# Optimization experiments

Measured on AMD Instinct MI355X. Metric: run time of the kernel, lower is better.

The kernel has to match this reference:

```python
import jax, jax.numpy as jnp
import numpy as np

H = W = 256
N_VERTS = 6890
N_FACES = 13776
CHUNK = 164            # 13776 = 84 * 164
N_CHUNKS = N_FACES // CHUNK
BIG = 1e9
EPS = 1e-8


def _project(cam, verts):
    # weak-perspective: s * (xy + t); flip y into image (raster) space
    xy = cam[:, None, 0:1] * (verts[:, :, :2] + cam[:, None, 1:3])
    return jnp.concatenate([xy[..., 0:1], -xy[..., 1:2], verts[:, :, 2:3]], axis=-1)  # [B,N,3]


def _rasterize(proj, faces):
    """Z-buffered rasterization. proj [B,N,3], faces [F,3] ->
    fim [B,P] int32 (face index, -1 = background), wim [B,P,3] barycentric weights."""
    B = proj.shape[0]
    P = H * W
    tri = proj[:, faces]                                   # [B,F,3,3]
    tri_c = tri.reshape(B, N_CHUNKS, CHUNK, 3, 3).transpose(1, 0, 2, 3, 4)  # [nc,B,C,3,3]
    bases = (jnp.arange(N_CHUNKS) * CHUNK).astype(jnp.int32)
    c = (jnp.arange(H, dtype=jnp.float32) + 0.5) / H * 2.0 - 1.0   # pixel centers in [-1,1]
    py, px = jnp.meshgrid(c, c, indexing='ij')
    px = px.reshape(-1)[None, :, None]                     # [1,P,1]
    py = py.reshape(-1)[None, :, None]

    def step(carry, xs):
        zbuf, fid, wim = carry
        t, base = xs                                       # t [B,CHUNK,3,3]
        v = t[:, None]                                     # [B,1,CHUNK,3,3]
        x0, y0, z0 = v[..., 0, 0], v[..., 0, 1], v[..., 0, 2]
        x1, y1, z1 = v[..., 1, 0], v[..., 1, 1], v[..., 1, 2]
        x2, y2, z2 = v[..., 2, 0], v[..., 2, 1], v[..., 2, 2]
        denom = (y1 - y2) * (x0 - x2) + (x2 - x1) * (y0 - y2)
        inv = 1.0 / jnp.where(jnp.abs(denom) < EPS, 1.0, denom)
        w0 = ((y1 - y2) * (px - x2) + (x2 - x1) * (py - y2)) * inv   # [B,P,CHUNK]
        w1 = ((y2 - y0) * (px - x2) + (x0 - x2) * (py - y2)) * inv
        w2 = 1.0 - w0 - w1
        inside = (w0 >= 0) & (w1 >= 0) & (w2 >= 0) & (jnp.abs(denom) >= EPS)
        depth = jnp.where(inside, w0 * z0 + w1 * z1 + w2 * z2, BIG)
        loc = jnp.argmin(depth, axis=-1)                   # [B,P]
        li = loc[..., None]
        dmin = jnp.take_along_axis(depth, li, -1)[..., 0]
        b0 = jnp.take_along_axis(w0, li, -1)[..., 0]
        b1 = jnp.take_along_axis(w1, li, -1)[..., 0]
        b2 = jnp.take_along_axis(w2, li, -1)[..., 0]
        bsel = jnp.stack([b0, b1, b2], axis=-1)            # [B,P,3]
        upd = dmin < zbuf
        zbuf = jnp.where(upd, dmin, zbuf)
        fid = jnp.where(upd, base + loc.astype(jnp.int32), fid)
        wim = jnp.where(upd[..., None], bsel, wim)
        return (zbuf, fid, wim), None

    init = (jnp.full((B, P), BIG, jnp.float32),
            jnp.full((B, P), -1, jnp.int32),
            jnp.zeros((B, P, 3), jnp.float32))
    (zbuf, fid, wim), _ = jax.lax.scan(step, init, (tri_c, bases))
    return fid, wim


def _grid_sample_border(img, grid):
    # torch.nn.functional.grid_sample(bilinear, padding_mode='border', align_corners=False)
    B, C, Hh, Ww = img.shape
    ix = jnp.clip(((grid[..., 0] + 1.0) * Ww - 1.0) * 0.5, 0.0, Ww - 1.0)
    iy = jnp.clip(((grid[..., 1] + 1.0) * Hh - 1.0) * 0.5, 0.0, Hh - 1.0)
    x0 = jnp.floor(ix); y0 = jnp.floor(iy)
    wx = ix - x0; wy = iy - y0
    x0i = x0.astype(jnp.int32); y0i = y0.astype(jnp.int32)
    x1i = jnp.clip(x0i + 1, 0, Ww - 1); y1i = jnp.clip(y0i + 1, 0, Hh - 1)
    b = jnp.arange(B)[:, None, None]
    Ia = img[b, :, y0i, x0i]   # [B,H,W,C]
    Ib = img[b, :, y0i, x1i]
    Ic = img[b, :, y1i, x0i]
    Id = img[b, :, y1i, x1i]
    out = (Ia * ((1 - wx) * (1 - wy))[..., None] + Ib * (wx * (1 - wy))[..., None]
           + Ic * ((1 - wx) * wy)[..., None] + Id * (wx * wy)[..., None])
    return out.transpose(0, 3, 1, 2)


def setup_inputs() -> dict:
    key = jax.random.key(0)
    k1, k2, k3, k4, k5, k6 = jax.random.split(key, 6)
    B = 2
    return {
        'src_img': jax.random.normal(k1, (B, 3, H, W), jnp.float32),
        'src_cam': jax.random.uniform(k2, (B, 3), jnp.float32),
        'src_vertices': jax.random.normal(k3, (B, N_VERTS, 3), jnp.float32),
        'tgt_cam': jax.random.uniform(k4, (B, 3), jnp.float32),
        'tgt_vertices': jax.random.normal(k5, (B, N_VERTS, 3), jnp.float32),
        'faces': jax.random.randint(k6, (N_FACES, 3), 0, N_VERTS, jnp.int32),
    }


def reference(src_img, src_cam, src_vertices, tgt_cam, tgt_vertices, faces):
    B = src_img.shape[0]
    # source faces -> projected 2D verts; flip y back (matches src_f2verts[...,1] *= -1)
    src_proj = _project(src_cam, src_vertices)
    src_f2v = src_proj[:, faces][..., 0:2]                 # [B,F,3,2]
    src_f2v = src_f2v.at[..., 1].multiply(-1.0)
    # rasterize target mesh -> face-index map + barycentric weight map
    tgt_proj = _project(tgt_cam, tgt_vertices)
    fim, wim = _rasterize(tgt_proj, faces)                 # [B,P], [B,P,3]
    fid_clip = jnp.clip(fim, 0, N_FACES - 1)
    gathered = src_f2v[jnp.arange(B)[:, None], fid_clip]   # [B,P,3,2]
    flow = jnp.sum(wim[..., None] * gathered, axis=2)      # [B,P,2]
    flow = jnp.where((fim >= 0)[..., None], flow, -2.0)    # background off-grid
    flow = flow.reshape(B, H, W, 2)
    return _grid_sample_border(src_img, flow)
```

## Files before the change

kernel.cpp:

```cpp
#include <hip/hip_runtime.h>

#pragma clang fp contract(off)

#define HH 256
#define WW 256
#define NVERTS 6890
#define NFACES 13776
#define RASTN (NFACES + 1)
#define PAD1 14336
#define LISTSTRIDE 13824
#define RCHUNK 32
#define MAXCH 432
#define KSPLIT 16
#define SLABS 4
#define WSUB 896
#define NITER 14
#define SLABSZ (4 * WSUB)
#define NBLK 2048
#define NWAVES (NBLK * 4)
#define BIGF 1000000000.0f
#define EPSF 1e-8f

__device__ __forceinline__ float pixc(int i) {
    return __fsub_rn(__fmul_rn(__fdiv_rn(__fadd_rn((float)i, 0.5f), 256.0f), 2.0f), 1.0f);
}

__device__ __forceinline__ unsigned int fsort(float f) {
    unsigned int u = __float_as_uint(f);
    return (u & 0x80000000u) ? ~u : (u | 0x80000000u);
}

__device__ __forceinline__ float funsort(unsigned int u) {
    if (u == 0xFFFFFFFFu) return BIGF;
    unsigned int v = (u & 0x80000000u) ? (u & 0x7FFFFFFFu) : ~u;
    return __uint_as_float(v);
}


__global__ __launch_bounds__(256) void precompute_kernel(
    const float* __restrict__ src_cam, const float* __restrict__ src_verts,
    const float* __restrict__ tgt_cam, const float* __restrict__ tgt_verts,
    const int* __restrict__ faces,
    float4* __restrict__ rast64, float* __restrict__ fz,
    uchar4* __restrict__ pass1,
    float4* __restrict__ eplane,
    float4* __restrict__ flowg,
    unsigned long long* __restrict__ zbuf,
    int* __restrict__ counts, int* __restrict__ done,
    int* __restrict__ qcountA, int* __restrict__ qcountB,
    int B)
{
    int idx = blockIdx.x * blockDim.x + threadIdx.x;
    if (idx < B * HH * WW) zbuf[idx] = ~0ull;
    if (counts && idx < B * 256) { counts[idx] = 0; done[idx] = 0; }
    if (qcountA && idx == 0) { qcountA[0] = 0; qcountB[0] = 0; }
    if (idx >= B * PAD1) return;
    int b = idx / PAD1;
    int f = idx - b * PAD1;
    if (f >= NFACES) {
        if (pass1) pass1[(size_t)b * PAD1 + f] = make_uchar4(255, 255, 0, 0);
        if (f == NFACES) {
            float4* rr = rast64 + ((size_t)b * RASTN + f) * 4;
            rr[0] = make_float4(0.0f, 0.0f, 0.0f, 0.0f);
            rr[1] = make_float4(0.0f, 0.0f, 1.0f, __int_as_float(-1));
            rr[2] = make_float4(BIGF, BIGF, BIGF, 0.0f);
            rr[3] = make_float4(0.0f, 0.0f, 0.0f, 0.0f);
            if (fz) fz[(size_t)b * RASTN + f] = BIGF;
        }
        return;
    }
    float4* rr = rast64 + ((size_t)b * RASTN + f) * 4;
    int i0 = faces[3*f+0], i1 = faces[3*f+1], i2 = faces[3*f+2];

    float tc0 = tgt_cam[3*b+0], tc1 = tgt_cam[3*b+1], tc2 = tgt_cam[3*b+2];
    const float* tv = tgt_verts + (size_t)b * NVERTS * 3;
    float x0 = __fmul_rn(tc0, __fadd_rn(tv[3*i0+0], tc1));
    float y0 = -__fmul_rn(tc0, __fadd_rn(tv[3*i0+1], tc2));
    float z0 = tv[3*i0+2];
    float x1 = __fmul_rn(tc0, __fadd_rn(tv[3*i1+0], tc1));
    float y1 = -__fmul_rn(tc0, __fadd_rn(tv[3*i1+1], tc2));
    float z1 = tv[3*i1+2];
    float x2 = __fmul_rn(tc0, __fadd_rn(tv[3*i2+0], tc1));
    float y2 = -__fmul_rn(tc0, __fadd_rn(tv[3*i2+1], tc2));
    float z2 = tv[3*i2+2];

    float A  = __fsub_rn(y1, y2);
    float D  = __fsub_rn(x0, x2);
    float Bc = __fsub_rn(x2, x1);
    float E_ = __fsub_rn(y0, y2);
    float denom = __fadd_rn(__fmul_rn(A, D), __fmul_rn(Bc, E_));
    bool valid = (fabsf(denom) >= EPSF);
    float inv = __fdiv_rn(1.0f, valid ? denom : 1.0f);
    float Cc = __fsub_rn(y2, y0);

    float fzmin = fminf(fminf(z0, z1), z2)
                - 4e-6f * (fabsf(z0) + fabsf(z1) + fabsf(z2)) - 1e-30f;

    if (valid) {
        rr[0] = make_float4(x2, y2, A, Bc);
        rr[1] = make_float4(Cc, D, inv, __int_as_float(f));
        rr[2] = make_float4(z0, z1, z2, 0.0f);
    } else {
        rr[0] = make_float4(0.0f, 0.0f, 0.0f, 0.0f);
        rr[1] = make_float4(0.0f, 0.0f, 1.0f, __int_as_float(f));
        rr[2] = make_float4(BIGF, BIGF, BIGF, 0.0f);
    }
    rr[3] = make_float4(0.0f, 0.0f, 0.0f, 0.0f);
    if (fz) fz[(size_t)b * RASTN + f] = valid ? fzmin : BIGF;

    uchar4 range;
    float4 e1, e2, e3;
    if (valid) {
        float xmn = fminf(fminf(x0, x1), x2), xmx = fmaxf(fmaxf(x0, x1), x2);
        float ymn = fminf(fminf(y0, y1), y2), ymx = fmaxf(fmaxf(y0, y1), y2);
        float S = fmaxf(fmaxf(fabsf(xmn), fabsf(xmx)),
                        fmaxf(fabsf(ymn), fabsf(ymx))) + 1.01f;
        float slop = 2e-6f * S;
        float l0 = sqrtf(D*D + E_*E_);
        float dx1v = x1 - x2, dy1v = y1 - y2;
        float l1 = sqrtf(dx1v*dx1v + dy1v*dy1v);
        float dx2v = x1 - x0, dy2v = y1 - y0;
        float l2 = sqrtf(dx2v*dx2v + dy2v*dy2v);
        float mp = fmaxf(fmaxf(l0*l1, l1*l2), l0*l2);
        float Ex = slop * mp / fabsf(denom);
        float m = Ex + slop + 1e-4f;
        float bxmn = xmn - m, bymn = ymn - m, bxmx = xmx + m, bymx = ymx + m;

        int txlo = (int)floorf((__fmul_rn(__fadd_rn(bxmn, 1.0f), 128.0f) - 15.5f) * 0.0625f);
        txlo = max(0, min(16, txlo));
        while (txlo > 0  && pixc(16*(txlo-1)+15) >= bxmn) txlo--;
        while (txlo < 16 && pixc(16*txlo+15)     <  bxmn) txlo++;
        int txhi = (int)floorf((__fmul_rn(__fadd_rn(bxmx, 1.0f), 128.0f) - 0.5f) * 0.0625f);
        txhi = max(-1, min(15, txhi));
        while (txhi < 15 && pixc(16*(txhi+1)) <= bxmx) txhi++;
        while (txhi >= 0 && pixc(16*txhi)     >  bxmx) txhi--;
        int tylo = (int)floorf((__fmul_rn(__fadd_rn(bymn, 1.0f), 128.0f) - 15.5f) * 0.0625f);
        tylo = max(0, min(16, tylo));
        while (tylo > 0  && pixc(16*(tylo-1)+15) >= bymn) tylo--;
        while (tylo < 16 && pixc(16*tylo+15)     <  bymn) tylo++;
        int tyhi = (int)floorf((__fmul_rn(__fadd_rn(bymx, 1.0f), 128.0f) - 0.5f) * 0.0625f);
        tyhi = max(-1, min(15, tyhi));
        while (tyhi < 15 && pixc(16*(tyhi+1)) <= bymx) tyhi++;
        while (tyhi >= 0 && pixc(16*tyhi)     >  bymx) tyhi--;
        if (txlo > txhi || tylo > tyhi || txlo > 15 || tylo > 15 ||
            txhi < 0 || tyhi < 0) {
            range = make_uchar4(255, 255, 0, 0);
        } else {
            range = make_uchar4((unsigned char)txlo, (unsigned char)tylo,
                                (unsigned char)txhi, (unsigned char)tyhi);
        }

        float s = (denom >= 0.0f) ? 1.0f : -1.0f;
        float gx0 = s * A,  gy0 = s * Bc;
        float gx1 = s * Cc, gy1 = s * D;
        float gx2 = s * (y0 - y1), gy2 = s * (x1 - x0);
        float b0 = -(gx0 * x2 + gy0 * y2);
        float b1 = -(gx1 * x2 + gy1 * y2);
        float b2 = fabsf(denom) - b0 - b1;
        float mm15 = 1.5f * m;
        float k0 = b0 + mm15 * l1 + 1e-6f;
        float k1 = b1 + mm15 * l0 + 1e-6f;
        float k2 = b2 + mm15 * l2 + 1e-6f;
        e1 = make_float4(gx0, gy0, k0, gx1);
        e2 = make_float4(gy1, k1, gx2, gy2);
        e3 = make_float4(k2, 0.0f, 0.0f, 0.0f);
    } else {
        range = make_uchar4(255, 255, 0, 0);
        e1 = make_float4(0.0f, 0.0f, -1.0f, 0.0f);
        e2 = make_float4(0.0f, -1.0f, 0.0f, 0.0f);
        e3 = make_float4(-1.0f, 0.0f, 0.0f, 0.0f);
    }
    if (pass1) pass1[(size_t)b * PAD1 + f] = range;
    if (eplane) {
        float4* ep = eplane + ((size_t)b * NFACES + f) * 4;
        ep[0] = e1; ep[1] = e2; ep[2] = e3;
        ep[3] = make_float4(0.0f, 0.0f, 0.0f, 0.0f);
    }

    float sc0 = src_cam[3*b+0], sc1 = src_cam[3*b+1], sc2 = src_cam[3*b+2];
    const float* sv = src_verts + (size_t)b * NVERTS * 3;
    float g0x = __fmul_rn(sc0, __fadd_rn(sv[3*i0+0], sc1));
    float g0y = __fmul_rn(sc0, __fadd_rn(sv[3*i0+1], sc2));
    float g1x = __fmul_rn(sc0, __fadd_rn(sv[3*i1+0], sc1));
    float g1y = __fmul_rn(sc0, __fadd_rn(sv[3*i1+1], sc2));
    float g2x = __fmul_rn(sc0, __fadd_rn(sv[3*i2+0], sc1));
    float g2y = __fmul_rn(sc0, __fadd_rn(sv[3*i2+1], sc2));
    size_t fo = ((size_t)b * NFACES + f) * 2;
    flowg[fo+0] = make_float4(g0x, g0y, g1x, g1y);
    flowg[fo+1] = make_float4(g2x, g2y, 0.0f, 0.0f);
}

__global__ __launch_bounds__(256) void bin_kernel(
    const uchar4* __restrict__ pass1, const float4* __restrict__ eplane,
    int* __restrict__ lists,
    int* __restrict__ counts, int* __restrict__ done,
    unsigned int* __restrict__ queueA, int* __restrict__ qcountA,
    unsigned int* __restrict__ queueB, int* __restrict__ qcountB, int B)
{
    __shared__ int seg[4][WSUB];
    int tile = blockIdx.x;
    int slab = blockIdx.y;
    int b = blockIdx.z;
    int tileG = b * 256 + tile;
    int tX = tile & 15, tY = tile >> 4;
    float txmin = pixc(tX * 16), txmax = pixc(tX * 16 + 15);
    float tymin = pixc(tY * 16), tymax = pixc(tY * 16 + 15);

    int wv = threadIdx.x >> 6, lane = threadIdx.x & 63;
    const uchar4* p1 = pass1 + (size_t)b * PAD1;
    const float4* ep = eplane + (size_t)b * NFACES * 4;
    int* mylist = lists + (size_t)tileG * LISTSTRIDE;
    int wlo = slab * SLABSZ + wv * WSUB;
    int cnt = 0;

    int f0 = wlo + lane;
    uchar4 c = p1[f0];

    #pragma unroll
    for (int it = 0; it < NITER; ++it) {
        uchar4 n;
        if (it + 1 < NITER) n = p1[f0 + (it + 1) * 64];
        int f = f0 + it * 64;
        bool pass = (tX >= (int)c.x) & (tX <= (int)c.z) &
                    (tY >= (int)c.y) & (tY <= (int)c.w);
        unsigned long long m = __ballot(pass);
        if (pass) {
            int pre = __popcll(m & ((1ull << lane) - 1ull));
            seg[wv][cnt + pre] = f;
        }
        cnt += __popcll(m);
        c = n;
    }

    int outc = 0;
    for (int base = 0; base < cnt; base += 64) {
        int i = base + lane;
        int f = (i < cnt) ? seg[wv][i] : 0;
        const float4* er = ep + (size_t)f * 4;
        float4 e1 = er[0], e2 = er[1], e3 = er[2];
        float v0 = e1.x * (e1.x >= 0.0f ? txmax : txmin)
                 + e1.y * (e1.y >= 0.0f ? tymax : tymin) + e1.z;
        float v1 = e1.w * (e1.w >= 0.0f ? txmax : txmin)
                 + e2.x * (e2.x >= 0.0f ? tymax : tymin) + e2.y;
        float v2 = e2.z * (e2.z >= 0.0f ? txmax : txmin)
                 + e2.w * (e2.w >= 0.0f ? tymax : tymin) + e3.x;
        bool pass = (i < cnt) & (v0 >= 0.0f) & (v1 >= 0.0f) & (v2 >= 0.0f);
        unsigned long long m = __ballot(pass);
        if (pass) {
            int pre = __popcll(m & ((1ull << lane) - 1ull));
            seg[wv][outc + pre] = f;
        }
        outc += __popcll(m);
    }
    cnt = outc;

    int gbase = 0;
    if (lane == 0 && cnt) gbase = atomicAdd(&counts[tileG], cnt);
    gbase = __shfl(gbase, 0);
    for (int i = lane; i < cnt; i += 64) mylist[gbase + i] = seg[wv][i];

    __syncthreads();
    if (threadIdx.x < 64) {
        int isLast = 0, cc = 0;
        if (threadIdx.x == 0) {
            isLast = (atomicAdd(&done[tileG], 1) == SLABS - 1);
            if (isLast) cc = atomicAdd(&counts[tileG], 0);
        }
        isLast = __shfl(isLast, 0);
        if (isLast) {
            cc = __shfl(cc, 0);
            int padded = (cc + RCHUNK - 1) & ~(RCHUNK - 1);
            for (int i = cc + threadIdx.x; i < padded; i += 64)
                mylist[i] = NFACES;
            int nch = padded / RCHUNK;
            int na = min(nch, KSPLIT);
            int nb = nch - na;
            if (na) {
                int qb = 0;
                if (threadIdx.x == 0) qb = atomicAdd(qcountA, na);
                qb = __shfl(qb, 0);
                for (int kk = threadIdx.x; kk < na; kk += 64)
                    queueA[qb + kk] =
                        ((unsigned int)tileG << 10) | (unsigned int)kk;
            }
            if (nb) {
                int qb = 0;
                if (threadIdx.x == 0) qb = atomicAdd(qcountB, nb);
                qb = __shfl(qb, 0);
                for (int kk = threadIdx.x; kk < nb; kk += 64)
                    queueB[qb + kk] =
                        ((unsigned int)tileG << 10) | (unsigned int)(KSPLIT + kk);
            }
        }
    }
}

__global__ __launch_bounds__(256) void raster_kernel(
    const float* __restrict__ rast64, const int* __restrict__ lists,
    const float* __restrict__ fz,
    const unsigned int* __restrict__ queue, const int* __restrict__ qcount,
    unsigned long long* __restrict__ zbuf, int B, int cull)
{
    int wv = threadIdx.x >> 6, lane = threadIdx.x & 63;
    int waveId = blockIdx.x * 4 + wv;
    int qn = queue ? qcount[0] : B * 256 * MAXCH;
    qn = __builtin_amdgcn_readfirstlane(qn);

    for (int e = waveId; e < qn; e += NWAVES) {
        int tileG, k;
        if (queue) {
            unsigned int ent = queue[e];
            tileG = (int)(ent >> 10); k = (int)(ent & 1023u);
        } else {
            tileG = e / MAXCH; k = e - tileG * MAXCH;
        }
        tileG = __builtin_amdgcn_readfirstlane(tileG);
        k = __builtin_amdgcn_readfirstlane(k);
        const int* lp = lists ? (lists + (size_t)tileG * LISTSTRIDE + k * RCHUNK)
                              : nullptr;
        int b = tileG >> 8, tile = tileG & 255;
        const float* rb = rast64 + (size_t)b * RASTN * 16;

        int tX = tile & 15, tY = tile >> 4;
        int col = lane & 15, row0 = lane >> 4;
        int pxi = tX * 16 + col;
        float px = pixc(pxi);
        int ry0 = tY * 16 + row0;
        float py0 = pixc(ry0);
        float py1 = pixc(ry0 + 4);
        float py2 = pixc(ry0 + 8);
        float py3 = pixc(ry0 + 12);

        float z0c = BIGF, z1c = BIGF, z2c = BIGF, z3c = BIGF;
        int f0c = -1, f1c = -1, f2c = -1, f3c = -1;

        if (cull && lp) {
            size_t zbase = ((size_t)b << 16) | (size_t)pxi;
            unsigned long long pk0 = zbuf[zbase | ((size_t)ry0 << 8)];
            unsigned long long pk1 = zbuf[zbase | ((size_t)(ry0 + 4) << 8)];
            unsigned long long pk2 = zbuf[zbase | ((size_t)(ry0 + 8) << 8)];
            unsigned long long pk3 = zbuf[zbase | ((size_t)(ry0 + 12) << 8)];
            float lb = fmaxf(fmaxf(funsort((unsigned int)(pk0 >> 32)),
                                   funsort((unsigned int)(pk1 >> 32))),
                             fmaxf(funsort((unsigned int)(pk2 >> 32)),
                                   funsort((unsigned int)(pk3 >> 32))));
            #pragma unroll
            for (int off = 1; off < 64; off <<= 1)
                lb = fmaxf(lb, __shfl_xor(lb, off, 64));
            int fidx = lp[lane & 31];
            float fzv = fz[(size_t)b * RASTN + fidx];
            unsigned long long bm = __ballot((lane < 32) & (fzv <= lb));
            unsigned int mask = (unsigned int)bm;
            if (mask == 0u) continue;

            for (int j = 0; j < RCHUNK; j += 4) {
                unsigned int g = (mask >> j) & 0xFu;
                if (!g) continue;
                int4 fis = *(const int4*)(lp + j);
                #pragma unroll
                for (int q = 0; q < 4; ++q) {
                    if (!(g & (1u << q))) continue;
                    int fi = (q == 0) ? fis.x : (q == 1) ? fis.y
                           : (q == 2) ? fis.z : fis.w;
                    fi = __builtin_amdgcn_readfirstlane(fi);
                    const float* r = rb + (size_t)fi * 16;
                    float X2 = r[0], Y2 = r[1], A = r[2], Bc = r[3];
                    float Cc = r[4], Dd = r[5], inv = r[6];
                    int   fid = __float_as_int(r[7]);
                    float Z0 = r[8], Z1 = r[9], Z2 = r[10];
                    float dx  = __fsub_rn(px, X2);
                    float Adx = __fmul_rn(A, dx);
                    float Cdx = __fmul_rn(Cc, dx);
                    auto evalp = [&](float py, float& zc, int& fc) {
                        float dy = __fsub_rn(py, Y2);
                        float w0 = __fmul_rn(__fadd_rn(Adx, __fmul_rn(Bc, dy)), inv);
                        float w1 = __fmul_rn(__fadd_rn(Cdx, __fmul_rn(Dd, dy)), inv);
                        float w2 = __fsub_rn(__fsub_rn(1.0f, w0), w1);
                        float d  = __fadd_rn(__fadd_rn(__fmul_rn(w0, Z0),
                                                       __fmul_rn(w1, Z1)),
                                             __fmul_rn(w2, Z2));
                        float mm = fminf(fminf(w0, w1), w2);
                        bool ins = (mm >= 0.0f) & (d < zc);
                        if (ins) { zc = d; fc = fid; }
                    };
                    evalp(py0, z0c, f0c);
                    evalp(py1, z1c, f1c);
                    evalp(py2, z2c, f2c);
                    evalp(py3, z3c, f3c);
                }
            }
        } else {
            for (int j = 0; j < RCHUNK; j += 4) {
                int4 fis;
                if (lp) {
                    fis = *(const int4*)(lp + j);
                } else {
                    int base = k * RCHUNK + j;
                    fis.x = min(base + 0, NFACES); fis.y = min(base + 1, NFACES);
                    fis.z = min(base + 2, NFACES); fis.w = min(base + 3, NFACES);
                }
                #pragma unroll
                for (int q = 0; q < 4; ++q) {
                    int fi = (q == 0) ? fis.x : (q == 1) ? fis.y
                           : (q == 2) ? fis.z : fis.w;
                    fi = __builtin_amdgcn_readfirstlane(fi);
                    const float* r = rb + (size_t)fi * 16;
                    float X2 = r[0], Y2 = r[1], A = r[2], Bc = r[3];
                    float Cc = r[4], Dd = r[5], inv = r[6];
                    int   fid = __float_as_int(r[7]);
                    float Z0 = r[8], Z1 = r[9], Z2 = r[10];
                    float dx  = __fsub_rn(px, X2);
                    float Adx = __fmul_rn(A, dx);
                    float Cdx = __fmul_rn(Cc, dx);
                    auto evalp = [&](float py, float& zc, int& fc) {
                        float dy = __fsub_rn(py, Y2);
                        float w0 = __fmul_rn(__fadd_rn(Adx, __fmul_rn(Bc, dy)), inv);
                        float w1 = __fmul_rn(__fadd_rn(Cdx, __fmul_rn(Dd, dy)), inv);
                        float w2 = __fsub_rn(__fsub_rn(1.0f, w0), w1);
                        float d  = __fadd_rn(__fadd_rn(__fmul_rn(w0, Z0),
                                                       __fmul_rn(w1, Z1)),
                                             __fmul_rn(w2, Z2));
                        float mm = fminf(fminf(w0, w1), w2);
                        bool ins = (mm >= 0.0f) & (d < zc);
                        if (ins) { zc = d; fc = fid; }
                    };
                    evalp(py0, z0c, f0c);
                    evalp(py1, z1c, f1c);
                    evalp(py2, z2c, f2c);
                    evalp(py3, z3c, f3c);
                }
            }
        }

        auto commit = [&](int rowk, float zc, int fc) {
            if (fc >= 0) {
                unsigned long long pk =
                    ((unsigned long long)fsort(zc) << 32) | (unsigned int)fc;
                int pyi = ry0 + rowk * 4;
                atomicMin(&zbuf[((size_t)b << 16) | (pyi << 8) | pxi], pk);
            }
        };
        commit(0, z0c, f0c);
        commit(1, z1c, f1c);
        commit(2, z2c, f2c);
        commit(3, z3c, f3c);
    }
}

__global__ __launch_bounds__(256) void resolve_kernel(
    const float* __restrict__ rast64, const float4* __restrict__ flowg,
    const unsigned long long* __restrict__ zbuf,
    const float* __restrict__ src_img, float* __restrict__ out, int B)
{
    int idx = blockIdx.x * 256 + threadIdx.x;
    if (idx >= B * HH * WW) return;
    int b = idx >> 16;
    int pix = idx & 65535;
    int pxi = pix & 255, pyi = pix >> 8;
    float px = pixc(pxi), py = pixc(pyi);

    unsigned int fid = (unsigned int)zbuf[idx];
    float fx, fy;
    if (fid != 0xFFFFFFFFu) {
        const float* r = rast64 + ((size_t)b * RASTN + fid) * 16;
        float dx = __fsub_rn(px, r[0]);
        float dy = __fsub_rn(py, r[1]);
        float w0 = __fmul_rn(__fadd_rn(__fmul_rn(r[2], dx), __fmul_rn(r[3], dy)), r[6]);
        float w1 = __fmul_rn(__fadd_rn(__fmul_rn(r[4], dx), __fmul_rn(r[5], dy)), r[6]);
        float w2 = __fsub_rn(__fsub_rn(1.0f, w0), w1);
        const float4* fg = flowg + ((size_t)b * NFACES + fid) * 2;
        float4 g0 = fg[0];
        float4 g1 = fg[1];
        fx = __fadd_rn(__fadd_rn(__fmul_rn(w0, g0.x), __fmul_rn(w1, g0.z)),
                       __fmul_rn(w2, g1.x));
        fy = __fadd_rn(__fadd_rn(__fmul_rn(w0, g0.y), __fmul_rn(w1, g0.w)),
                       __fmul_rn(w2, g1.y));
    } else {
        fx = -2.0f; fy = -2.0f;
    }

    float ix = __fmul_rn(__fsub_rn(__fmul_rn(__fadd_rn(fx, 1.0f), 256.0f), 1.0f), 0.5f);
    float iy = __fmul_rn(__fsub_rn(__fmul_rn(__fadd_rn(fy, 1.0f), 256.0f), 1.0f), 0.5f);
    ix = fminf(fmaxf(ix, 0.0f), 255.0f);
    iy = fminf(fmaxf(iy, 0.0f), 255.0f);
    float x0f = floorf(ix), y0f = floorf(iy);
    float wx = __fsub_rn(ix, x0f), wy = __fsub_rn(iy, y0f);
    int x0i = (int)x0f, y0i = (int)y0f;
    int x1i = min(x0i + 1, 255), y1i = min(y0i + 1, 255);
    float omwx = __fsub_rn(1.0f, wx), omwy = __fsub_rn(1.0f, wy);
    float wa = __fmul_rn(omwx, omwy);
    float wb = __fmul_rn(wx, omwy);
    float wc = __fmul_rn(omwx, wy);
    float wd = __fmul_rn(wx, wy);
    const float* img = src_img + (size_t)b * 3 * HH * WW;
    int o00 = y0i * WW + x0i, o01 = y0i * WW + x1i;
    int o10 = y1i * WW + x0i, o11 = y1i * WW + x1i;
    float* ob = out + (size_t)b * 3 * HH * WW + (size_t)pyi * WW + pxi;
    for (int c = 0; c < 3; ++c) {
        const float* ic = img + (size_t)c * HH * WW;
        float Ia = ic[o00], Ib = ic[o01], Ic = ic[o10], Id = ic[o11];
        float val = __fadd_rn(__fadd_rn(__fadd_rn(__fmul_rn(Ia, wa), __fmul_rn(Ib, wb)),
                                        __fmul_rn(Ic, wc)),
                              __fmul_rn(Id, wd));
        ob[(size_t)c * HH * WW] = val;
    }
}

extern "C" void kernel_launch(void* const* d_in, const int* in_sizes, int n_in,
                              void* d_out, int out_size, void* d_ws, size_t ws_size,
                              hipStream_t stream)
{
    const float* src_img   = (const float*)d_in[0];
    const float* src_cam   = (const float*)d_in[1];
    const float* src_verts = (const float*)d_in[2];
    const float* tgt_cam   = (const float*)d_in[3];
    const float* tgt_verts = (const float*)d_in[4];
    const int*   faces     = (const int*)d_in[5];
    int B = in_sizes[1] / 3;

    size_t off = 0;
    auto alloc = [&](size_t bytes) {
        size_t o = off;
        off = (off + bytes + 255) & ~(size_t)255;
        return o;
    };
    size_t rastOff = alloc((size_t)B * RASTN * 64);
    size_t fzOff   = alloc((size_t)B * RASTN * sizeof(float));
    size_t p1Off   = alloc((size_t)B * PAD1 * 4);
    size_t edgOff  = alloc((size_t)B * NFACES * 64);
    size_t flowOff = alloc((size_t)B * NFACES * 2 * sizeof(float4));
    size_t zbufOff = alloc((size_t)B * HH * WW * sizeof(unsigned long long));
    size_t cntOff  = alloc((size_t)B * 256 * sizeof(int));
    size_t donOff  = alloc((size_t)B * 256 * sizeof(int));
    size_t qcAOff  = alloc(sizeof(int));
    size_t qcBOff  = alloc(sizeof(int));
    size_t quAOff  = alloc((size_t)B * 256 * KSPLIT * sizeof(unsigned int));
    size_t quBOff  = alloc((size_t)B * 256 * MAXCH * sizeof(unsigned int));
    size_t listOff = alloc((size_t)B * 256 * LISTSTRIDE * sizeof(int));
    bool binned = (off <= ws_size);

    char* ws = (char*)d_ws;
    float4* rast64 = (float4*)(ws + rastOff);
    float*  fz     = (float*)(ws + fzOff);
    uchar4* pass1  = binned ? (uchar4*)(ws + p1Off)  : nullptr;
    float4* eplane = binned ? (float4*)(ws + edgOff) : nullptr;
    float4* flowg  = (float4*)(ws + flowOff);
    unsigned long long* zbuf = (unsigned long long*)(ws + zbufOff);
    int* counts = binned ? (int*)(ws + cntOff) : nullptr;
    int* done   = binned ? (int*)(ws + donOff) : nullptr;
    int* qcountA = binned ? (int*)(ws + qcAOff) : nullptr;
    int* qcountB = binned ? (int*)(ws + qcBOff) : nullptr;
    unsigned int* queueA = binned ? (unsigned int*)(ws + quAOff) : nullptr;
    unsigned int* queueB = binned ? (unsigned int*)(ws + quBOff) : nullptr;
    int* lists  = binned ? (int*)(ws + listOff) : nullptr;

    int nInit = B * HH * WW;
    int nPre  = B * PAD1;
    int nMax  = nInit > nPre ? nInit : nPre;
    precompute_kernel<<<(nMax + 255) / 256, 256, 0, stream>>>(
        src_cam, src_verts, tgt_cam, tgt_verts, faces,
        rast64, fz, pass1, eplane, flowg, zbuf, counts, done,
        qcountA, qcountB, B);
    if (binned) {
        bin_kernel<<<dim3(256, SLABS, B), 256, 0, stream>>>(
            pass1, eplane, lists, counts, done,
            queueA, qcountA, queueB, qcountB, B);
        raster_kernel<<<NBLK, 256, 0, stream>>>(
            (const float*)rast64, lists, fz, queueA, qcountA, zbuf, B, 0);
        raster_kernel<<<NBLK, 256, 0, stream>>>(
            (const float*)rast64, lists, fz, queueB, qcountB, zbuf, B, 1);
    } else {
        raster_kernel<<<NBLK, 256, 0, stream>>>(
            (const float*)rast64, nullptr, fz, nullptr, nullptr, zbuf, B, 0);
    }
    resolve_kernel<<<(B * HH * WW + 255) / 256, 256, 0, stream>>>(
        (const float*)rast64, flowg, zbuf, src_img, (float*)d_out, B);
}
```

Before: 140.1 us.

## Replace tile-parallel binning with face-parallel count/prefix/scatter binning

```diff
diff --git a/kernel.cpp b/kernel.cpp
--- a/kernel.cpp
+++ b/kernel.cpp
@@ -7,17 +7,13 @@
 #define NVERTS 6890
 #define NFACES 13776
 #define RASTN (NFACES + 1)
-#define PAD1 14336
 #define LISTSTRIDE 13824
 #define RCHUNK 32
 #define MAXCH 432
 #define KSPLIT 16
-#define SLABS 4
-#define WSUB 896
-#define NITER 14
-#define SLABSZ (4 * WSUB)
 #define NBLK 2048
 #define NWAVES (NBLK * 4)
+#define MAXB 4
 #define BIGF 1000000000.0f
 #define EPSF 1e-8f
 
@@ -42,34 +38,27 @@
     const float* __restrict__ tgt_cam, const float* __restrict__ tgt_verts,
     const int* __restrict__ faces,
     float4* __restrict__ rast64, float* __restrict__ fz,
-    uchar4* __restrict__ pass1,
-    float4* __restrict__ eplane,
+    float4* __restrict__ binrec,
     float4* __restrict__ flowg,
     unsigned long long* __restrict__ zbuf,
-    int* __restrict__ counts, int* __restrict__ done,
     int* __restrict__ qcountA, int* __restrict__ qcountB,
     int B)
 {
     int idx = blockIdx.x * blockDim.x + threadIdx.x;
     if (idx < B * HH * WW) zbuf[idx] = ~0ull;
-    if (counts && idx < B * 256) { counts[idx] = 0; done[idx] = 0; }
     if (qcountA && idx == 0) { qcountA[0] = 0; qcountB[0] = 0; }
-    if (idx >= B * PAD1) return;
-    int b = idx / PAD1;
-    int f = idx - b * PAD1;
-    if (f >= NFACES) {
-        if (pass1) pass1[(size_t)b * PAD1 + f] = make_uchar4(255, 255, 0, 0);
-        if (f == NFACES) {
-            float4* rr = rast64 + ((size_t)b * RASTN + f) * 4;
-            rr[0] = make_float4(0.0f, 0.0f, 0.0f, 0.0f);
-            rr[1] = make_float4(0.0f, 0.0f, 1.0f, __int_as_float(-1));
-            rr[2] = make_float4(BIGF, BIGF, BIGF, 0.0f);
-            rr[3] = make_float4(0.0f, 0.0f, 0.0f, 0.0f);
-            if (fz) fz[(size_t)b * RASTN + f] = BIGF;
-        }
+    if (idx >= B * RASTN) return;
+    int b = idx / RASTN;
+    int f = idx - b * RASTN;
+    float4* rr = rast64 + ((size_t)b * RASTN + f) * 4;
+    if (f == NFACES) {
+        rr[0] = make_float4(0.0f, 0.0f, 0.0f, 0.0f);
+        rr[1] = make_float4(0.0f, 0.0f, 1.0f, __int_as_float(-1));
+        rr[2] = make_float4(BIGF, BIGF, BIGF, 0.0f);
+        rr[3] = make_float4(0.0f, 0.0f, 0.0f, 0.0f);
+        if (fz) fz[(size_t)b * RASTN + f] = BIGF;
         return;
     }
-    float4* rr = rast64 + ((size_t)b * RASTN + f) * 4;
     int i0 = faces[3*f+0], i1 = faces[3*f+1], i2 = faces[3*f+2];
 
     float tc0 = tgt_cam[3*b+0], tc1 = tgt_cam[3*b+1], tc2 = tgt_cam[3*b+2];
@@ -108,8 +97,9 @@
     rr[3] = make_float4(0.0f, 0.0f, 0.0f, 0.0f);
     if (fz) fz[(size_t)b * RASTN + f] = valid ? fzmin : BIGF;
 
-    uchar4 range;
-    float4 e1, e2, e3;
+    unsigned int rngbits = 255u | (255u << 8);
+    float4 e1, e2;
+    float k2v = -1.0f;
     if (valid) {
         float xmn = fminf(fminf(x0, x1), x2), xmx = fmaxf(fmaxf(x0, x1), x2);
         float ymn = fminf(fminf(y0, y1), y2), ymx = fmaxf(fmaxf(y0, y1), y2);
@@ -142,13 +132,11 @@
         tyhi = max(-1, min(15, tyhi));
         while (tyhi < 15 && pixc(16*(tyhi+1)) <= bymx) tyhi++;
         while (tyhi >= 0 && pixc(16*tyhi)     >  bymx) tyhi--;
-        if (txlo > txhi || tylo > tyhi || txlo > 15 || tylo > 15 ||
-            txhi < 0 || tyhi < 0) {
-            range = make_uchar4(255, 255, 0, 0);
-        } else {
-            range = make_uchar4((unsigned char)txlo, (unsigned char)tylo,
-                                (unsigned char)txhi, (unsigned char)tyhi);
-        }
+        bool hasRange = !(txlo > txhi || tylo > tyhi || txlo > 15 || tylo > 15 ||
+                          txhi < 0 || tyhi < 0);
+        if (hasRange)
+            rngbits = (unsigned)txlo | ((unsigned)tylo << 8)
+                    | ((unsigned)txhi << 16) | ((unsigned)tyhi << 24);
 
         float s = (denom >= 0.0f) ? 1.0f : -1.0f;
         float gx0 = s * A,  gy0 = s * Bc;
@@ -160,21 +148,19 @@
         float mm15 = 1.5f * m;
         float k0 = b0 + mm15 * l1 + 1e-6f;
         float k1 = b1 + mm15 * l0 + 1e-6f;
-        float k2 = b2 + mm15 * l2 + 1e-6f;
+        k2v = b2 + mm15 * l2 + 1e-6f;
         e1 = make_float4(gx0, gy0, k0, gx1);
         e2 = make_float4(gy1, k1, gx2, gy2);
-        e3 = make_float4(k2, 0.0f, 0.0f, 0.0f);
     } else {
-        range = make_uchar4(255, 255, 0, 0);
         e1 = make_float4(0.0f, 0.0f, -1.0f, 0.0f);
         e2 = make_float4(0.0f, -1.0f, 0.0f, 0.0f);
-        e3 = make_float4(-1.0f, 0.0f, 0.0f, 0.0f);
-    }
-    if (pass1) pass1[(size_t)b * PAD1 + f] = range;
-    if (eplane) {
-        float4* ep = eplane + ((size_t)b * NFACES + f) * 4;
-        ep[0] = e1; ep[1] = e2; ep[2] = e3;
-        ep[3] = make_float4(0.0f, 0.0f, 0.0f, 0.0f);
+    }
+    if (binrec) {
+        size_t ps = (size_t)B * NFACES;
+        size_t fi = (size_t)b * NFACES + f;
+        binrec[fi]          = e1;
+        binrec[ps + fi]     = e2;
+        binrec[2*ps + fi]   = make_float4(k2v, __uint_as_float(rngbits), 0.0f, 0.0f);
     }
 
     float sc0 = src_cam[3*b+0], sc1 = src_cam[3*b+1], sc2 = src_cam[3*b+2];
@@ -190,106 +176,111 @@
     flowg[fo+1] = make_float4(g2x, g2y, 0.0f, 0.0f);
 }
 
-__global__ __launch_bounds__(256) void bin_kernel(
-    const uchar4* __restrict__ pass1, const float4* __restrict__ eplane,
-    int* __restrict__ lists,
-    int* __restrict__ counts, int* __restrict__ done,
+__global__ __launch_bounds__(256) void bin_count_kernel(
+    const float4* __restrict__ binrec, int* __restrict__ blockCnt, int B)
+{
+    __shared__ int cnt[MAXB * 256];
+    int NT = B * 256;
+    for (int t = threadIdx.x; t < NT; t += 256) cnt[t] = 0;
+    __syncthreads();
+    int idx = blockIdx.x * 256 + threadIdx.x;
+    if (idx < B * NFACES) {
+        size_t ps = (size_t)B * NFACES;
+        float4 p0 = binrec[idx], p1 = binrec[ps + idx], p2 = binrec[2*ps + idx];
+        unsigned int r = __float_as_uint(p2.y);
+        int txlo = r & 255, tylo = (r >> 8) & 255;
+        int txhi = (r >> 16) & 255, tyhi = (r >> 24) & 255;
+        int b = idx / NFACES;
+        for (int ty = tylo; ty <= tyhi; ++ty) {
+            float tymin = pixc(ty*16), tymax = pixc(ty*16 + 15);
+            float vy0 = p0.y * (p0.y >= 0.0f ? tymax : tymin);
+            float vy1 = p1.x * (p1.x >= 0.0f ? tymax : tymin);
+            float vy2 = p1.w * (p1.w >= 0.0f ? tymax : tymin);
+            for (int tx = txlo; tx <= txhi; ++tx) {
+                float txmin = pixc(tx*16), txmax = pixc(tx*16 + 15);
+                float v0 = p0.x * (p0.x >= 0.0f ? txmax : txmin) + vy0 + p0.z;
+                float v1 = p0.w * (p0.w >= 0.0f ? txmax : txmin) + vy1 + p1.y;
+                float v2 = p1.z * (p1.z >= 0.0f ? txmax : txmin) + vy2 + p2.x;
+                if ((v0 >= 0.0f) & (v1 >= 0.0f) & (v2 >= 0.0f))
+                    atomicAdd(&cnt[b * 256 + ty * 16 + tx], 1);
+            }
+        }
+    }
+    __syncthreads();
+    for (int t = threadIdx.x; t < NT; t += 256)
+        blockCnt[(size_t)blockIdx.x * NT + t] = cnt[t];
+}
+
+__global__ __launch_bounds__(256) void bin_prefix_kernel(
+    int* __restrict__ blockCnt, int* __restrict__ lists,
     unsigned int* __restrict__ queueA, int* __restrict__ qcountA,
-    unsigned int* __restrict__ queueB, int* __restrict__ qcountB, int B)
-{
-    __shared__ int seg[4][WSUB];
-    int tile = blockIdx.x;
-    int slab = blockIdx.y;
-    int b = blockIdx.z;
-    int tileG = b * 256 + tile;
-    int tX = tile & 15, tY = tile >> 4;
-    float txmin = pixc(tX * 16), txmax = pixc(tX * 16 + 15);
-    float tymin = pixc(tY * 16), tymax = pixc(tY * 16 + 15);
-
-    int wv = threadIdx.x >> 6, lane = threadIdx.x & 63;
-    const uchar4* p1 = pass1 + (size_t)b * PAD1;
-    const float4* ep = eplane + (size_t)b * NFACES * 4;
+    unsigned int* __restrict__ queueB, int* __restrict__ qcountB,
+    int nBlk, int B)
+{
+    int tileG = blockIdx.x;
+    int NT = B * 256;
+    __shared__ int s_total, s_qbA, s_qbB;
+    if (threadIdx.x == 0) {
+        int run = 0;
+        for (int blk = 0; blk < nBlk; ++blk) {
+            int c = blockCnt[(size_t)blk * NT + tileG];
+            blockCnt[(size_t)blk * NT + tileG] = run;
+            run += c;
+        }
+        s_total = run;
+        int padded = (run + RCHUNK - 1) & ~(RCHUNK - 1);
+        int nch = padded / RCHUNK;
+        int na = min(nch, KSPLIT);
+        int nb = nch - na;
+        s_qbA = na ? atomicAdd(qcountA, na) : 0;
+        s_qbB = nb ? atomicAdd(qcountB, nb) : 0;
+    }
+    __syncthreads();
+    int total = s_total;
+    int padded = (total + RCHUNK - 1) & ~(RCHUNK - 1);
     int* mylist = lists + (size_t)tileG * LISTSTRIDE;
-    int wlo = slab * SLABSZ + wv * WSUB;
-    int cnt = 0;
-
-    int f0 = wlo + lane;
-    uchar4 c = p1[f0];
-
-    #pragma unroll
-    for (int it = 0; it < NITER; ++it) {
-        uchar4 n;
-        if (it + 1 < NITER) n = p1[f0 + (it + 1) * 64];
-        int f = f0 + it * 64;
-        bool pass = (tX >= (int)c.x) & (tX <= (int)c.z) &
-                    (tY >= (int)c.y) & (tY <= (int)c.w);
-        unsigned long long m = __ballot(pass);
-        if (pass) {
-            int pre = __popcll(m & ((1ull << lane) - 1ull));
-            seg[wv][cnt + pre] = f;
-        }
-        cnt += __popcll(m);
-        c = n;
-    }
-
-    int outc = 0;
-    for (int base = 0; base < cnt; base += 64) {
-        int i = base + lane;
-        int f = (i < cnt) ? seg[wv][i] : 0;
-        const float4* er = ep + (size_t)f * 4;
-        float4 e1 = er[0], e2 = er[1], e3 = er[2];
-        float v0 = e1.x * (e1.x >= 0.0f ? txmax : txmin)
-                 + e1.y * (e1.y >= 0.0f ? tymax : tymin) + e1.z;
-        float v1 = e1.w * (e1.w >= 0.0f ? txmax : txmin)
-                 + e2.x * (e2.x >= 0.0f ? tymax : tymin) + e2.y;
-        float v2 = e2.z * (e2.z >= 0.0f ? txmax : txmin)
-                 + e2.w * (e2.w >= 0.0f ? tymax : tymin) + e3.x;
-        bool pass = (i < cnt) & (v0 >= 0.0f) & (v1 >= 0.0f) & (v2 >= 0.0f);
-        unsigned long long m = __ballot(pass);
-        if (pass) {
-            int pre = __popcll(m & ((1ull << lane) - 1ull));
-            seg[wv][outc + pre] = f;
-        }
-        outc += __popcll(m);
-    }
-    cnt = outc;
-
-    int gbase = 0;
-    if (lane == 0 && cnt) gbase = atomicAdd(&counts[tileG], cnt);
-    gbase = __shfl(gbase, 0);
-    for (int i = lane; i < cnt; i += 64) mylist[gbase + i] = seg[wv][i];
-
+    for (int i = total + threadIdx.x; i < padded; i += 256) mylist[i] = NFACES;
+    int nch = padded / RCHUNK;
+    int na = min(nch, KSPLIT), nb = nch - na;
+    for (int kk = threadIdx.x; kk < na; kk += 256)
+        queueA[s_qbA + kk] = ((unsigned int)tileG << 10) | (unsigned int)kk;
+    for (int kk = threadIdx.x; kk < nb; kk += 256)
+        queueB[s_qbB + kk] = ((unsigned int)tileG << 10) | (unsigned int)(KSPLIT + kk);
+}
+
+__global__ __launch_bounds__(256) void bin_scatter_kernel(
+    const float4* __restrict__ binrec, const int* __restrict__ blockCnt,
+    int* __restrict__ lists, int B)
+{
+    __shared__ int cur[MAXB * 256];
+    int NT = B * 256;
+    for (int t = threadIdx.x; t < NT; t += 256)
+        cur[t] = blockCnt[(size_t)blockIdx.x * NT + t];
     __syncthreads();
-    if (threadIdx.x < 64) {
-        int isLast = 0, cc = 0;
-        if (threadIdx.x == 0) {
-            isLast = (atomicAdd(&done[tileG], 1) == SLABS - 1);
-            if (isLast) cc = atomicAdd(&counts[tileG], 0);
-        }
-        isLast = __shfl(isLast, 0);
-        if (isLast) {
-            cc = __shfl(cc, 0);
-            int padded = (cc + RCHUNK - 1) & ~(RCHUNK - 1);
-            for (int i = cc + threadIdx.x; i < padded; i += 64)
-                mylist[i] = NFACES;
-            int nch = padded / RCHUNK;
-            int na = min(nch, KSPLIT);
-            int nb = nch - na;
-            if (na) {
-                int qb = 0;
-                if (threadIdx.x == 0) qb = atomicAdd(qcountA, na);
-                qb = __shfl(qb, 0);
-                for (int kk = threadIdx.x; kk < na; kk += 64)
-                    queueA[qb + kk] =
-                        ((unsigned int)tileG << 10) | (unsigned int)kk;
-            }
-            if (nb) {
-                int qb = 0;
-                if (threadIdx.x == 0) qb = atomicAdd(qcountB, nb);
-                qb = __shfl(qb, 0);
-                for (int kk = threadIdx.x; kk < nb; kk += 64)
-                    queueB[qb + kk] =
-                        ((unsigned int)tileG << 10) | (unsigned int)(KSPLIT + kk);
+    int idx = blockIdx.x * 256 + threadIdx.x;
+    if (idx < B * NFACES) {
+        size_t ps = (size_t)B * NFACES;
+        float4 p0 = binrec[idx], p1 = binrec[ps + idx], p2 = binrec[2*ps + idx];
+        unsigned int r = __float_as_uint(p2.y);
+        int txlo = r & 255, tylo = (r >> 8) & 255;
+        int txhi = (r >> 16) & 255, tyhi = (r >> 24) & 255;
+        int b = idx / NFACES;
+        int f = idx - b * NFACES;
+        for (int ty = tylo; ty <= tyhi; ++ty) {
+            float tymin = pixc(ty*16), tymax = pixc(ty*16 + 15);
+            float vy0 = p0.y * (p0.y >= 0.0f ? tymax : tymin);
+            float vy1 = p1.x * (p1.x >= 0.0f ? tymax : tymin);
+            float vy2 = p1.w * (p1.w >= 0.0f ? tymax : tymin);
+            for (int tx = txlo; tx <= txhi; ++tx) {
+                float txmin = pixc(tx*16), txmax = pixc(tx*16 + 15);
+                float v0 = p0.x * (p0.x >= 0.0f ? txmax : txmin) + vy0 + p0.z;
+                float v1 = p0.w * (p0.w >= 0.0f ? txmax : txmin) + vy1 + p1.y;
+                float v2 = p1.z * (p1.z >= 0.0f ? txmax : txmin) + vy2 + p2.x;
+                if ((v0 >= 0.0f) & (v1 >= 0.0f) & (v2 >= 0.0f)) {
+                    int tg = b * 256 + ty * 16 + tx;
+                    int pos = atomicAdd(&cur[tg], 1);
+                    lists[(size_t)tg * LISTSTRIDE + pos] = f;
+                }
             }
         }
     }
@@ -517,6 +508,7 @@
     const float* tgt_verts = (const float*)d_in[4];
     const int*   faces     = (const int*)d_in[5];
     int B = in_sizes[1] / 3;
+    int nBlk = (B * NFACES + 255) / 256;
 
     size_t off = 0;
     auto alloc = [&](size_t bytes) {
@@ -526,28 +518,24 @@
     };
     size_t rastOff = alloc((size_t)B * RASTN * 64);
     size_t fzOff   = alloc((size_t)B * RASTN * sizeof(float));
-    size_t p1Off   = alloc((size_t)B * PAD1 * 4);
-    size_t edgOff  = alloc((size_t)B * NFACES * 64);
+    size_t brOff   = alloc((size_t)B * NFACES * 3 * sizeof(float4));
+    size_t bcOff   = alloc((size_t)nBlk * B * 256 * sizeof(int));
     size_t flowOff = alloc((size_t)B * NFACES * 2 * sizeof(float4));
     size_t zbufOff = alloc((size_t)B * HH * WW * sizeof(unsigned long long));
-    size_t cntOff  = alloc((size_t)B * 256 * sizeof(int));
-    size_t donOff  = alloc((size_t)B * 256 * sizeof(int));
     size_t qcAOff  = alloc(sizeof(int));
     size_t qcBOff  = alloc(sizeof(int));
     size_t quAOff  = alloc((size_t)B * 256 * KSPLIT * sizeof(unsigned int));
     size_t quBOff  = alloc((size_t)B * 256 * MAXCH * sizeof(unsigned int));
     size_t listOff = alloc((size_t)B * 256 * LISTSTRIDE * sizeof(int));
-    bool binned = (off <= ws_size);
+    bool binned = (off <= ws_size) && (B <= MAXB);
 
     char* ws = (char*)d_ws;
     float4* rast64 = (float4*)(ws + rastOff);
     float*  fz     = (float*)(ws + fzOff);
-    uchar4* pass1  = binned ? (uchar4*)(ws + p1Off)  : nullptr;
-    float4* eplane = binned ? (float4*)(ws + edgOff) : nullptr;
+    float4* binrec = binned ? (float4*)(ws + brOff) : nullptr;
+    int* blockCnt  = binned ? (int*)(ws + bcOff) : nullptr;
     float4* flowg  = (float4*)(ws + flowOff);
     unsigned long long* zbuf = (unsigned long long*)(ws + zbufOff);
-    int* counts = binned ? (int*)(ws + cntOff) : nullptr;
-    int* done   = binned ? (int*)(ws + donOff) : nullptr;
     int* qcountA = binned ? (int*)(ws + qcAOff) : nullptr;
     int* qcountB = binned ? (int*)(ws + qcBOff) : nullptr;
     unsigned int* queueA = binned ? (unsigned int*)(ws + quAOff) : nullptr;
@@ -555,16 +543,16 @@
     int* lists  = binned ? (int*)(ws + listOff) : nullptr;
 
     int nInit = B * HH * WW;
-    int nPre  = B * PAD1;
+    int nPre  = B * RASTN;
     int nMax  = nInit > nPre ? nInit : nPre;
     precompute_kernel<<<(nMax + 255) / 256, 256, 0, stream>>>(
         src_cam, src_verts, tgt_cam, tgt_verts, faces,
-        rast64, fz, pass1, eplane, flowg, zbuf, counts, done,
-        qcountA, qcountB, B);
+        rast64, fz, binrec, flowg, zbuf, qcountA, qcountB, B);
     if (binned) {
-        bin_kernel<<<dim3(256, SLABS, B), 256, 0, stream>>>(
-            pass1, eplane, lists, counts, done,
-            queueA, qcountA, queueB, qcountB, B);
+        bin_count_kernel<<<nBlk, 256, 0, stream>>>(binrec, blockCnt, B);
+        bin_prefix_kernel<<<B * 256, 256, 0, stream>>>(
+            blockCnt, lists, queueA, qcountA, queueB, qcountB, nBlk, B);
+        bin_scatter_kernel<<<nBlk, 256, 0, stream>>>(binrec, blockCnt, lists, B);
         raster_kernel<<<NBLK, 256, 0, stream>>>(
             (const float*)rast64, lists, fz, queueA, qcountA, zbuf, B, 0);
         raster_kernel<<<NBLK, 256, 0, stream>>>(
```

Result: slower. 180.7 us (+29.0%).

## Bin faces into 2x2 tile groups per block to share the coarse scan

Applied to the files above, without the earlier changes.

```diff
diff --git a/kernel.cpp b/kernel.cpp
--- a/kernel.cpp
+++ b/kernel.cpp
@@ -198,18 +198,23 @@
     unsigned int* __restrict__ queueB, int* __restrict__ qcountB, int B)
 {
     __shared__ int seg[4][WSUB];
-    int tile = blockIdx.x;
+    int grp = blockIdx.x;
     int slab = blockIdx.y;
     int b = blockIdx.z;
-    int tileG = b * 256 + tile;
-    int tX = tile & 15, tY = tile >> 4;
-    float txmin = pixc(tX * 16), txmax = pixc(tX * 16 + 15);
-    float tymin = pixc(tY * 16), tymax = pixc(tY * 16 + 15);
+    int gx = grp & 7, gy = grp >> 3;
+    int tx0 = gx * 2, ty0 = gy * 2;
+    float txmn[2], txmx[2], tymn[2], tymx[2];
+    #pragma unroll
+    for (int t = 0; t < 2; ++t) {
+        txmn[t] = pixc((tx0 + t) * 16);
+        txmx[t] = pixc((tx0 + t) * 16 + 15);
+        tymn[t] = pixc((ty0 + t) * 16);
+        tymx[t] = pixc((ty0 + t) * 16 + 15);
+    }
 
     int wv = threadIdx.x >> 6, lane = threadIdx.x & 63;
     const uchar4* p1 = pass1 + (size_t)b * PAD1;
     const float4* ep = eplane + (size_t)b * NFACES * 4;
-    int* mylist = lists + (size_t)tileG * LISTSTRIDE;
     int wlo = slab * SLABSZ + wv * WSUB;
     int cnt = 0;
 
@@ -221,8 +226,8 @@
         uchar4 n;
         if (it + 1 < NITER) n = p1[f0 + (it + 1) * 64];
         int f = f0 + it * 64;
-        bool pass = (tX >= (int)c.x) & (tX <= (int)c.z) &
-                    (tY >= (int)c.y) & (tY <= (int)c.w);
+        bool pass = ((int)c.x <= tx0 + 1) & ((int)c.z >= tx0) &
+                    ((int)c.y <= ty0 + 1) & ((int)c.w >= ty0);
         unsigned long long m = __ballot(pass);
         if (pass) {
             int pre = __popcll(m & ((1ull << lane) - 1ull));
@@ -232,64 +237,86 @@
         c = n;
     }
 
-    int outc = 0;
     for (int base = 0; base < cnt; base += 64) {
         int i = base + lane;
-        int f = (i < cnt) ? seg[wv][i] : 0;
+        bool alive = (i < cnt);
+        int f = alive ? seg[wv][i] : 0;
+        uchar4 rg = p1[f];
         const float4* er = ep + (size_t)f * 4;
         float4 e1 = er[0], e2 = er[1], e3 = er[2];
-        float v0 = e1.x * (e1.x >= 0.0f ? txmax : txmin)
-                 + e1.y * (e1.y >= 0.0f ? tymax : tymin) + e1.z;
-        float v1 = e1.w * (e1.w >= 0.0f ? txmax : txmin)
-                 + e2.x * (e2.x >= 0.0f ? tymax : tymin) + e2.y;
-        float v2 = e2.z * (e2.z >= 0.0f ? txmax : txmin)
-                 + e2.w * (e2.w >= 0.0f ? tymax : tymin) + e3.x;
-        bool pass = (i < cnt) & (v0 >= 0.0f) & (v1 >= 0.0f) & (v2 >= 0.0f);
-        unsigned long long m = __ballot(pass);
-        if (pass) {
-            int pre = __popcll(m & ((1ull << lane) - 1ull));
-            seg[wv][outc + pre] = f;
-        }
-        outc += __popcll(m);
-    }
-    cnt = outc;
-
-    int gbase = 0;
-    if (lane == 0 && cnt) gbase = atomicAdd(&counts[tileG], cnt);
-    gbase = __shfl(gbase, 0);
-    for (int i = lane; i < cnt; i += 64) mylist[gbase + i] = seg[wv][i];
+        float x0p[2], x1p[2], x2p[2], y0p[2], y1p[2], y2p[2];
+        #pragma unroll
+        for (int t = 0; t < 2; ++t) {
+            x0p[t] = e1.x * (e1.x >= 0.0f ? txmx[t] : txmn[t]);
+            x1p[t] = e1.w * (e1.w >= 0.0f ? txmx[t] : txmn[t]);
+            x2p[t] = e2.z * (e2.z >= 0.0f ? txmx[t] : txmn[t]);
+            y0p[t] = e1.y * (e1.y >= 0.0f ? tymx[t] : tymn[t]);
+            y1p[t] = e2.x * (e2.x >= 0.0f ? tymx[t] : tymn[t]);
+            y2p[t] = e2.w * (e2.w >= 0.0f ? tymx[t] : tymn[t]);
+        }
+        #pragma unroll
+        for (int tt = 0; tt < 4; ++tt) {
+            int rx = tt & 1, ry = tt >> 1;
+            int tX = tx0 + rx, tY = ty0 + ry;
+            float v0 = x0p[rx] + y0p[ry] + e1.z;
+            float v1 = x1p[rx] + y1p[ry] + e2.y;
+            float v2 = x2p[rx] + y2p[ry] + e3.x;
+            bool pass = alive &
+                        ((int)rg.x <= tX) & ((int)rg.z >= tX) &
+                        ((int)rg.y <= tY) & ((int)rg.w >= tY) &
+                        (v0 >= 0.0f) & (v1 >= 0.0f) & (v2 >= 0.0f);
+            unsigned long long m = __ballot(pass);
+            int nn = __popcll(m);
+            if (nn) {
+                int tileG = b * 256 + tY * 16 + tX;
+                int gb = 0;
+                if (lane == 0) gb = atomicAdd(&counts[tileG], nn);
+                gb = __shfl(gb, 0);
+                if (pass) {
+                    int pre = __popcll(m & ((1ull << lane) - 1ull));
+                    lists[(size_t)tileG * LISTSTRIDE + gb + pre] = f;
+                }
+            }
+        }
+    }
 
     __syncthreads();
     if (threadIdx.x < 64) {
-        int isLast = 0, cc = 0;
-        if (threadIdx.x == 0) {
-            isLast = (atomicAdd(&done[tileG], 1) == SLABS - 1);
-            if (isLast) cc = atomicAdd(&counts[tileG], 0);
-        }
-        isLast = __shfl(isLast, 0);
-        if (isLast) {
-            cc = __shfl(cc, 0);
-            int padded = (cc + RCHUNK - 1) & ~(RCHUNK - 1);
-            for (int i = cc + threadIdx.x; i < padded; i += 64)
-                mylist[i] = NFACES;
-            int nch = padded / RCHUNK;
-            int na = min(nch, KSPLIT);
-            int nb = nch - na;
-            if (na) {
-                int qb = 0;
-                if (threadIdx.x == 0) qb = atomicAdd(qcountA, na);
-                qb = __shfl(qb, 0);
-                for (int kk = threadIdx.x; kk < na; kk += 64)
-                    queueA[qb + kk] =
-                        ((unsigned int)tileG << 10) | (unsigned int)kk;
+        #pragma unroll
+        for (int tt = 0; tt < 4; ++tt) {
+            int tX = tx0 + (tt & 1), tY = ty0 + (tt >> 1);
+            int tileG = b * 256 + tY * 16 + tX;
+            int isLast = 0, cc = 0;
+            if (threadIdx.x == 0) {
+                isLast = (atomicAdd(&done[tileG], 1) == SLABS - 1);
+                if (isLast) cc = atomicAdd(&counts[tileG], 0);
             }
-            if (nb) {
-                int qb = 0;
-                if (threadIdx.x == 0) qb = atomicAdd(qcountB, nb);
-                qb = __shfl(qb, 0);
-                for (int kk = threadIdx.x; kk < nb; kk += 64)
-                    queueB[qb + kk] =
-                        ((unsigned int)tileG << 10) | (unsigned int)(KSPLIT + kk);
+            isLast = __shfl(isLast, 0);
+            if (isLast) {
+                cc = __shfl(cc, 0);
+                int padded = (cc + RCHUNK - 1) & ~(RCHUNK - 1);
+                int* mylist = lists + (size_t)tileG * LISTSTRIDE;
+                for (int i2 = cc + threadIdx.x; i2 < padded; i2 += 64)
+                    mylist[i2] = NFACES;
+                int nch = padded / RCHUNK;
+                int na = min(nch, KSPLIT);
+                int nb2 = nch - na;
+                if (na) {
+                    int qb = 0;
+                    if (threadIdx.x == 0) qb = atomicAdd(qcountA, na);
+                    qb = __shfl(qb, 0);
+                    for (int kk = threadIdx.x; kk < na; kk += 64)
+                        queueA[qb + kk] =
+                            ((unsigned int)tileG << 10) | (unsigned int)kk;
+                }
+                if (nb2) {
+                    int qb = 0;
+                    if (threadIdx.x == 0) qb = atomicAdd(qcountB, nb2);
+                    qb = __shfl(qb, 0);
+                    for (int kk = threadIdx.x; kk < nb2; kk += 64)
+                        queueB[qb + kk] =
+                            ((unsigned int)tileG << 10) | (unsigned int)(KSPLIT + kk);
+                }
             }
         }
     }
@@ -562,7 +589,7 @@
         rast64, fz, pass1, eplane, flowg, zbuf, counts, done,
         qcountA, qcountB, B);
     if (binned) {
-        bin_kernel<<<dim3(256, SLABS, B), 256, 0, stream>>>(
+        bin_kernel<<<dim3(64, SLABS, B), 256, 0, stream>>>(
             pass1, eplane, lists, counts, done,
             queueA, qcountA, queueB, qcountB, B);
         raster_kernel<<<NBLK, 256, 0, stream>>>(
```

New measurement: 157.5 us. +12.4%, slower.
